# Kernel tuning notes

Hardware: AMD Instinct MI355X
Metric: run time of the kernel (lower is better)

Reference implementation:

```python
import jax, jax.numpy as jnp
import numpy as np

B, S, D_MODEL = 2, 2048, 2048
NUM_HEADS, NUM_KV_HEADS, HEAD_DIM = 16, 4, 128
MAX_SEQ = 2048
ROPE_WAVELENGTH = 10000.0


def apply_rope(x, positions, head_dim, max_wavelength):
    # x: [B, S, H, D], positions: [B, S]
    fraction = 2.0 * jnp.arange(0, head_dim // 2, dtype=jnp.float32) / head_dim
    timescale = max_wavelength ** fraction                      # [D/2]
    sinusoid = positions[..., None].astype(jnp.float32) / timescale  # [B,S,D/2]
    sin = jnp.sin(sinusoid)[:, :, None, :]                      # [B,S,1,D/2]
    cos = jnp.cos(sinusoid)[:, :, None, :]
    x1, x2 = jnp.split(x, 2, axis=-1)
    first = x1 * cos - x2 * sin
    second = x2 * cos + x1 * sin
    return jnp.concatenate([first, second], axis=-1).astype(x.dtype)


def setup_inputs() -> dict:
    key = jax.random.key(0)
    ks = jax.random.split(key, 5)
    inputs = jax.random.normal(ks[0], (B, S, D_MODEL), dtype=jnp.float32)
    seq_pos = jnp.broadcast_to(jnp.arange(S, dtype=jnp.int32)[None, :], (B, S))
    std = 0.01  # nnx.initializers.normal() default stddev
    wq = jax.random.normal(ks[1], (D_MODEL, NUM_HEADS, HEAD_DIM), dtype=jnp.float32) * std
    bq = jnp.zeros((NUM_HEADS, HEAD_DIM), dtype=jnp.float32)
    wkv = jax.random.normal(ks[2], (D_MODEL, NUM_KV_HEADS, 2 * HEAD_DIM), dtype=jnp.float32) * std
    bkv = jnp.zeros((NUM_KV_HEADS, 2 * HEAD_DIM), dtype=jnp.float32)
    wo = jax.random.normal(ks[3], (NUM_HEADS, HEAD_DIM, D_MODEL), dtype=jnp.float32) * std
    bo = jnp.zeros((D_MODEL,), dtype=jnp.float32)
    return {"inputs": inputs, "seq_pos": seq_pos, "wq": wq, "bq": bq,
            "wkv": wkv, "bkv": bkv, "wo": wo, "bo": bo}


def reference(inputs, seq_pos, wq, bq, wkv, bkv, wo, bo):
    dtype = inputs.dtype
    # Projections
    kv = jnp.einsum('bsd,dkh->bskh', inputs, wkv) + bkv          # [B,S,KV,2*HD]
    key, value = jnp.split(kv, 2, axis=-1)                       # [B,S,KV,HD] each
    query = jnp.einsum('bsd,dnh->bsnh', inputs, wq) + bq         # [B,S,H,HD]
    # RoPE
    query = apply_rope(query, seq_pos, HEAD_DIM, ROPE_WAVELENGTH)
    key = apply_rope(key, seq_pos, HEAD_DIM, ROPE_WAVELENGTH)
    # GQA: repeat KV heads
    rep = NUM_HEADS // NUM_KV_HEADS
    key_r = jnp.repeat(key, rep, axis=2)                          # [B,S,H,HD]
    value_r = jnp.repeat(value, rep, axis=2)
    # Attention (einsum_attention path)
    q = query / jnp.sqrt(jnp.asarray(HEAD_DIM, dtype=dtype))
    attn = jnp.einsum('bqhd,bkhd->bhqk', q, key_r)               # [B,H,S,S]
    # position_mask: seq_range <= time_steps -> causal
    seq_range = jnp.arange(MAX_SEQ, dtype=jnp.int32)
    mask = (seq_range[None, None, :] <= seq_pos[:, :, None])[:, None, :, :]  # [B,1,S,S]
    big_neg = jnp.finfo(dtype).min
    attn = jnp.where(mask, attn, big_neg)
    attn = jax.nn.softmax(attn, axis=-1).astype(dtype)
    x = jnp.einsum('bhqk,bkhd->bqhd', attn, value_r)             # [B,S,H,HD]
    out = jnp.einsum('bqhd,hdo->bqo', x, wo) + bo                # [B,S,D]
    return out
```

## Files before the change

### kernel.cpp

```cpp
#include <hip/hip_runtime.h>
#include <hip/hip_bf16.h>

#define DM    2048
#define SEQ   2048
#define NB    2
#define NH    16
#define NKVH  4
#define HD    128
#define NQKV  3072
#define MROWS 4096
#define KVB   64
#define QSC   0.08838834764831845f

using f32x4  = __attribute__((ext_vector_type(4))) float;
using f32x16 = __attribute__((ext_vector_type(16))) float;
using short8 = __attribute__((ext_vector_type(8))) short;
using ushort8 = __attribute__((ext_vector_type(8))) unsigned short;
using uint2v = __attribute__((ext_vector_type(2))) unsigned int;

static __device__ __forceinline__ unsigned short f2bf(float f) {
  __hip_bfloat16 h = __float2bfloat16(f);
  return *reinterpret_cast<unsigned short*>(&h);
}
static __device__ __forceinline__ float bf2f(unsigned short u) {
  union { unsigned int i; float f; } v; v.i = ((unsigned int)u) << 16; return v.f;
}
static __device__ __forceinline__ unsigned cvtpk_bf16(float lo, float hi) {
  unsigned r;
  asm("v_cvt_pk_bf16_f32 %0, %1, %2" : "=v"(r) : "v"(lo), "v"(hi));
  return r;
}

typedef __attribute__((address_space(1))) const unsigned char as1_c;
typedef __attribute__((address_space(3))) unsigned char as3_c;
static __device__ __forceinline__ void gload_lds16(const void* g, void* l) {
  __builtin_amdgcn_global_load_lds((as1_c*)g, (as3_c*)l, 16, 0, 0);
}


__global__ void build_trig(float2* __restrict__ tbl) {
  int i = blockIdx.x * 256 + threadIdx.x;
  int p = i >> 6, d = i & 63;
  float inv_ts = powf(10000.0f, -(float)d * (1.0f / 64.0f));
  float ang = (float)p * inv_ts;
  float sn, cs;
  sincosf(ang, &sn, &cs);
  tbl[i] = make_float2(cs, sn);
}


__global__ void f32_to_bf16_vec(const float* __restrict__ src, unsigned short* __restrict__ dst, int n4) {
  int i = blockIdx.x * blockDim.x + threadIdx.x;
  if (i < n4) {
    float4 v = reinterpret_cast<const float4*>(src)[i];
    ushort4 o;
    o.x = f2bf(v.x); o.y = f2bf(v.y); o.z = f2bf(v.z); o.w = f2bf(v.w);
    reinterpret_cast<ushort4*>(dst)[i] = o;
  }
}

__global__ void transpose_all(const float* __restrict__ wq, const float* __restrict__ wkv,
                              const float* __restrict__ wo,
                              unsigned short* __restrict__ WqkvT, unsigned short* __restrict__ WoT) {
  int bx = blockIdx.x;
  const float* src; unsigned short* dst; int N;
  if (bx < 64)       { src = wq;  dst = WqkvT;                         N = 2048; }
  else if (bx < 96)  { src = wkv; dst = WqkvT + (size_t)2048 * DM;     N = 1024; bx -= 64; }
  else               { src = wo;  dst = WoT;                           N = 2048; bx -= 96; }
  __shared__ float t[32][33];
  int n0 = bx * 32, k0 = blockIdx.y * 32;
  int tx = threadIdx.x, ty = threadIdx.y;
  for (int j = 0; j < 4; j++)
    t[ty + j * 8][tx] = src[(size_t)(k0 + ty + j * 8) * N + n0 + tx];
  __syncthreads();
  for (int j = 0; j < 4; j++)
    dst[(size_t)(n0 + ty + j * 8) * DM + k0 + tx] = f2bf(t[tx][ty + j * 8]);
}

__global__ void bias_concat(const float* __restrict__ bq, const float* __restrict__ bkv, float* __restrict__ o) {
  int i = blockIdx.x * 256 + threadIdx.x;
  if (i < NQKV) o[i] = (i < DM) ? bq[i] : bkv[i - DM];
}


#define STA(buf, kt, q) gload_lds16(gA + (size_t)((q) * 32) * K + (kt), LW + (buf) * 65536 + ((q) * 32 + rowA) * 128)
#define STB(buf, kt, h) gload_lds16(gB + (size_t)((h) * 64) * K + (kt), LW + (buf) * 65536 + 32768 + ((h) * 64 + rowB) * 128)

#define RDB(buf) \
  _Pragma("unroll") for (int ni = 0; ni < 4; ++ni) { \
    int row_ = (EPI == 1) ? (wc * 16 + ni * 64 + ln) : (wc * 64 + ni * 16 + ln); \
    const char* p_ = (const char*)LW + (buf) * 65536 + 32768 + row_ * 128; \
    bfr[ni][0] = *(const short8*)(p_ + coff0); \
    bfr[ni][1] = *(const short8*)(p_ + coff1); }

#define RDA(buf, q) \
  _Pragma("unroll") for (int m2 = 0; m2 < 2; ++m2) { \
    int row_ = wr * 128 + ((q) * 2 + m2) * 16 + ln; \
    const char* p_ = (const char*)LW + (buf) * 65536 + row_ * 128; \
    af[m2][0] = *(const short8*)(p_ + coff0); \
    af[m2][1] = *(const short8*)(p_ + coff1); }

#define MFQ(q) \
  _Pragma("unroll") for (int m2 = 0; m2 < 2; ++m2) \
  _Pragma("unroll") for (int ni = 0; ni < 4; ++ni) { \
    acc[(q) * 2 + m2][ni] = __builtin_amdgcn_mfma_f32_16x16x32_bf16(af[m2][0], bfr[ni][0], acc[(q) * 2 + m2][ni], 0, 0, 0); \
    acc[(q) * 2 + m2][ni] = __builtin_amdgcn_mfma_f32_16x16x32_bf16(af[m2][1], bfr[ni][1], acc[(q) * 2 + m2][ni], 0, 0, 0); }

#define SYNC_IN() do { __builtin_amdgcn_sched_barrier(0); __builtin_amdgcn_s_barrier(); \
  asm volatile("s_waitcnt lgkmcnt(0)" ::: "memory"); __builtin_amdgcn_sched_barrier(0); \
  __builtin_amdgcn_s_setprio(1); } while (0)
#define SYNC_OUT() do { __builtin_amdgcn_s_setprio(0); __builtin_amdgcn_sched_barrier(0); \
  __builtin_amdgcn_s_barrier(); } while (0)
#define SYNC_OUT_VM() do { __builtin_amdgcn_s_setprio(0); \
  asm volatile("s_waitcnt vmcnt(6)" ::: "memory"); __builtin_amdgcn_sched_barrier(0); \
  __builtin_amdgcn_s_barrier(); } while (0)

template <int EPI>
__global__ __launch_bounds__(512, 2) void gemm8(
    const unsigned short* __restrict__ A, const unsigned short* __restrict__ Bt,
    const float* __restrict__ bias, const int* __restrict__ seq_pos,
    const float2* __restrict__ tbl,
    unsigned short* __restrict__ Qo, unsigned short* __restrict__ Ko,
    unsigned short* __restrict__ Vo, float* __restrict__ Cout,
    int nbx, int N, int K) {
  __shared__ __align__(16) unsigned short lds[2 * 2 * 16384];
  int tid = threadIdx.x, lane = tid & 63, w = tid >> 6;
  int wr = w >> 2, wc = w & 3;
  int lg = lane >> 4, ln = lane & 15;

  int bid = blockIdx.x;
  int cpx = gridDim.x >> 3;
  int swz = (bid & 7) * cpx + (bid >> 3);
  int by = swz / nbx, bx = swz - by * nbx;
  int m0 = by * 256, n0 = bx * 256;

  int soff = ((lane & 7) ^ (lane >> 3)) << 3;
  const unsigned short* gA = A + (size_t)(m0 + ((w & 3) << 3) + ((w >> 2) << 7) + (lane >> 3)) * K + soff;
  const unsigned short* gB = Bt + (size_t)(n0 + (w << 3) + (lane >> 3)) * K + soff;
  char* LW = (char*)lds;
  int rowA = ((w & 3) << 3) + ((w >> 2) << 7);
  int rowB = (w << 3);
  int coff0 = ((lg)     ^ (ln & 7)) << 4;
  int coff1 = ((lg + 4) ^ (ln & 7)) << 4;

  f32x4 acc[8][4];
#pragma unroll
  for (int mi = 0; mi < 8; ++mi)
#pragma unroll
    for (int ni = 0; ni < 4; ++ni) acc[mi][ni] = (f32x4){0, 0, 0, 0};

  short8 bfr[4][2], af[2][2];

  STB(0, 0, 0); STB(0, 0, 1); STB(0, 0, 2); STB(0, 0, 3);
  STA(0, 0, 0); STA(0, 0, 1); STA(0, 0, 2); STA(0, 0, 3);
  STB(1, 64, 0); STB(1, 64, 1); STB(1, 64, 2); STB(1, 64, 3);
  STA(1, 64, 0); STA(1, 64, 1);
  asm volatile("s_waitcnt vmcnt(6)" ::: "memory");
  __builtin_amdgcn_sched_barrier(0);
  __builtin_amdgcn_s_barrier();

  for (int it = 0; it < (K >> 7); ++it) {
    int kt1  = it * 128 + 64;
    int ktn0 = (it * 128 + 128) & (K - 1);
    int ktn1 = (it * 128 + 192) & (K - 1);
    RDB(0); RDA(0, 0);
    STA(1, kt1, 2); STA(1, kt1, 3);
    SYNC_IN(); MFQ(0); SYNC_OUT();
    RDA(0, 1);
    STB(0, ktn0, 0); STB(0, ktn0, 1);
    SYNC_IN(); MFQ(1); SYNC_OUT();
    RDA(0, 2);
    STB(0, ktn0, 2); STB(0, ktn0, 3);
    SYNC_IN(); MFQ(2); SYNC_OUT();
    RDA(0, 3);
    STA(0, ktn0, 0); STA(0, ktn0, 1);
    SYNC_IN(); MFQ(3); SYNC_OUT_VM();
    RDB(1); RDA(1, 0);
    STA(0, ktn0, 2); STA(0, ktn0, 3);
    SYNC_IN(); MFQ(0); SYNC_OUT();
    RDA(1, 1);
    STB(1, ktn1, 0); STB(1, ktn1, 1);
    SYNC_IN(); MFQ(1); SYNC_OUT();
    RDA(1, 2);
    STB(1, ktn1, 2); STB(1, ktn1, 3);
    SYNC_IN(); MFQ(2); SYNC_OUT();
    RDA(1, 3);
    STA(1, ktn1, 0); STA(1, ktn1, 1);
    SYNC_IN(); MFQ(3); SYNC_OUT_VM();
  }
  asm volatile("s_waitcnt vmcnt(0)" ::: "memory");

  if constexpr (EPI == 0) {
#pragma unroll
    for (int mi = 0; mi < 8; ++mi) {
      int row = m0 + wr * 128 + mi * 16 + lg * 4;
#pragma unroll
      for (int ni = 0; ni < 4; ++ni) {
        int col = n0 + wc * 64 + ni * 16 + ln;
        float bv = bias[col];
#pragma unroll
        for (int r = 0; r < 4; ++r)
          Cout[(size_t)(row + r) * N + col] = acc[mi][ni][r] + bv;
      }
    }
  } else {
    int d = wc * 16 + ln;
    float bv0 = bias[n0 + d],      bv1 = bias[n0 + d + 64];
    float bv2 = bias[n0 + d + 128], bv3 = bias[n0 + d + 192];
    int bI = m0 >> 11, s0 = m0 & (SEQ - 1);
    int nt = n0 >> 8;
    if (nt < 8) {
      unsigned short* qp0 = Qo + (size_t)(bI * NH + nt * 2) * SEQ * HD;
      unsigned short* qp1 = qp0 + (size_t)SEQ * HD;
#pragma unroll
      for (int mi = 0; mi < 8; ++mi) {
        int sl = wr * 128 + mi * 16 + lg * 4;
#pragma unroll
        for (int r = 0; r < 4; ++r) {
          int s = s0 + sl + r;
          int pos = seq_pos[bI * SEQ + s];
          float2 cs = tbl[pos * 64 + d];
          float x1 = acc[mi][0][r] + bv0, x2 = acc[mi][1][r] + bv1;
          float y1 = acc[mi][2][r] + bv2, y2 = acc[mi][3][r] + bv3;
          unsigned short* q0 = qp0 + (size_t)s * HD;
          q0[d]      = f2bf((x1 * cs.x - x2 * cs.y) * QSC);
          q0[d + 64] = f2bf((x2 * cs.x + x1 * cs.y) * QSC);
          unsigned short* q1 = qp1 + (size_t)s * HD;
          q1[d]      = f2bf((y1 * cs.x - y2 * cs.y) * QSC);
          q1[d + 64] = f2bf((y2 * cs.x + y1 * cs.y) * QSC);
        }
      }
    } else {
      int kvh = nt - 8;
      unsigned short* kp = Ko + (size_t)(bI * NKVH + kvh) * SEQ * HD;
      unsigned short* vp = Vo + (size_t)(bI * NKVH + kvh) * HD * SEQ;
#pragma unroll
      for (int mi = 0; mi < 8; ++mi) {
        int sl = wr * 128 + mi * 16 + lg * 4;
        ushort4 v0q, v1q;
#pragma unroll
        for (int r = 0; r < 4; ++r) {
          int s = s0 + sl + r;
          int pos = seq_pos[bI * SEQ + s];
          float2 cs = tbl[pos * 64 + d];
          float x1 = acc[mi][0][r] + bv0, x2 = acc[mi][1][r] + bv1;
          unsigned short* krow = kp + (size_t)s * HD;
          krow[d]      = f2bf(x1 * cs.x - x2 * cs.y);
          krow[d + 64] = f2bf(x2 * cs.x + x1 * cs.y);
          ((unsigned short*)&v0q)[r] = f2bf(acc[mi][2][r] + bv2);
          ((unsigned short*)&v1q)[r] = f2bf(acc[mi][3][r] + bv3);
        }
        *(ushort4*)(vp + (size_t)d * SEQ + s0 + sl)        = v0q;
        *(ushort4*)(vp + (size_t)(d + 64) * SEQ + s0 + sl) = v1q;
      }
    }
  }
}


__global__ __launch_bounds__(256, 2) void flash_attn(const unsigned short* __restrict__ Q,
                                                     const unsigned short* __restrict__ Kr,
                                                     const unsigned short* __restrict__ Vt,
                                                     const int* __restrict__ seq_pos,
                                                     unsigned short* __restrict__ X) {
  __shared__ __align__(16) unsigned short lds_k[64 * 128];
  __shared__ __align__(16) unsigned short lds_v[128 * 64];
  int tid = threadIdx.x, lane = tid & 63, w = tid >> 6;
  int hi = lane >> 5, q5 = lane & 31;
  int bh = blockIdx.y, b = bh >> 4, h = bh & 15, kvhh = h >> 2;
  int qtile = 15 - (int)blockIdx.x;
  int qbase = qtile * 128;
  int q_global = qbase + w * 32 + q5;

  const unsigned short* kbase = Kr + ((size_t)(b * NKVH + kvhh)) * SEQ * HD;
  const unsigned short* vbase = Vt + ((size_t)(b * NKVH + kvhh)) * HD * SEQ;

  const unsigned short* gks[4]; unsigned short* lks[4];
  const unsigned short* gvs[4]; unsigned short* lvs[4];
#pragma unroll
  for (int i = 0; i < 4; i++) {
    int kr = w * 16 + i * 4 + (lane >> 4);
    int kc = (lane & 15) ^ (kr & 7);
    gks[i] = kbase + (size_t)kr * HD + kc * 8;
    lks[i] = lds_k + (w * 16 + i * 4) * 128;
    int vr = w * 32 + i * 8 + (lane >> 3);
    int vc = (lane & 7) ^ (vr & 7);
    gvs[i] = vbase + (size_t)vr * SEQ + vc * 8;
    lvs[i] = lds_v + (w * 32 + i * 8) * 64;
  }

  int pm = max(seq_pos[b * SEQ + qbase + lane], seq_pos[b * SEQ + qbase + 64 + lane]);
#pragma unroll
  for (int o = 32; o; o >>= 1) { int t2 = __shfl_xor(pm, o); pm = pm > t2 ? pm : t2; }
  int ntiles = (pm + KVB) >> 6;
  if (ntiles > SEQ / KVB) ntiles = SEQ / KVB;

  int pos_q = seq_pos[b * SEQ + q_global];
  int wmin = pos_q;
#pragma unroll
  for (int o = 32; o; o >>= 1) { int t2 = __shfl_xor(wmin, o); wmin = wmin < t2 ? wmin : t2; }

  short8 qf[8];
  {
    const unsigned short* qp = Q + ((size_t)((b * NH + h) * SEQ + q_global)) * HD + hi * 8;
#pragma unroll
    for (int c = 0; c < 8; c++) qf[c] = *reinterpret_cast<const short8*>(qp + c * 16);
  }

  f32x16 acc[4];
#pragma unroll
  for (int db = 0; db < 4; db++)
#pragma unroll
    for (int r = 0; r < 16; ++r) acc[db][r] = 0.0f;
  float m_q = -1e30f, l_q = 0.0f;

  const char* kp0 = (const char*)lds_k + q5 * 256;
  const char* kp1 = kp0 + 32 * 256;
  int swk = (q5 & 7) << 4;

  for (int t = 0; t < ntiles; t++) {
    int kv0 = t * KVB;
#pragma unroll
    for (int i = 0; i < 4; i++) {
      gload_lds16(gks[i] + (size_t)kv0 * HD, lks[i]);
      gload_lds16(gvs[i] + kv0, lvs[i]);
    }
    __syncthreads();

    f32x16 st0, st1;
#pragma unroll
    for (int r = 0; r < 16; ++r) { st0[r] = 0.0f; st1[r] = 0.0f; }
    __builtin_amdgcn_s_setprio(1);
#pragma unroll
    for (int c = 0; c < 8; c++) {
      short8 kf0 = *reinterpret_cast<const short8*>(kp0 + ((c * 32 + hi * 16) ^ swk));
      short8 kf1 = *reinterpret_cast<const short8*>(kp1 + ((c * 32 + hi * 16) ^ swk));
      st0 = __builtin_amdgcn_mfma_f32_32x32x16_bf16(kf0, qf[c], st0, 0, 0, 0);
      st1 = __builtin_amdgcn_mfma_f32_32x32x16_bf16(kf1, qf[c], st1, 0, 0, 0);
    }
    __builtin_amdgcn_s_setprio(0);

    if (kv0 + 63 > wmin) {
      int kvb = kv0 + 4 * hi;
#pragma unroll
      for (int r = 0; r < 16; ++r) {
        int kg = kvb + (r & 3) + 8 * (r >> 2);
        if (kg > pos_q)      st0[r] = -1e30f;
        if (kg + 32 > pos_q) st1[r] = -1e30f;
      }
    }

    float tm[16];
#pragma unroll
    for (int r = 0; r < 16; ++r) tm[r] = fmaxf(st0[r], st1[r]);
#pragma unroll
    for (int s = 8; s; s >>= 1)
#pragma unroll
      for (int r = 0; r < s; ++r) tm[r] = fmaxf(tm[r], tm[r + s]);
    float mx = fmaxf(tm[0], __shfl_xor(tm[0], 32));

    bool skip = (mx <= m_q + 8.0f) && (m_q > -1e29f);
    if (!__all((int)skip)) {
      float nm = fmaxf(m_q, mx);
      float corr = __expf(m_q - nm);
      m_q = nm; l_q *= corr;
#pragma unroll
      for (int db = 0; db < 4; db++)
#pragma unroll
        for (int r = 0; r < 16; ++r) acc[db][r] *= corr;
    }

    float sm[16];
#pragma unroll
    for (int r = 0; r < 16; ++r) {
      st0[r] = __expf(st0[r] - m_q);
      st1[r] = __expf(st1[r] - m_q);
      sm[r] = st0[r] + st1[r];
    }
#pragma unroll
    for (int s = 8; s; s >>= 1)
#pragma unroll
      for (int r = 0; r < s; ++r) sm[r] += sm[r + s];
    l_q += sm[0] + __shfl_xor(sm[0], 32);

    short8 pb[4];
#define MKFRAG(STV, B, OUT) { \
    unsigned a_ = cvtpk_bf16(STV[(B) + 0], STV[(B) + 1]); \
    unsigned b_ = cvtpk_bf16(STV[(B) + 2], STV[(B) + 3]); \
    unsigned c_ = cvtpk_bf16(STV[(B) + 4], STV[(B) + 5]); \
    unsigned d_ = cvtpk_bf16(STV[(B) + 6], STV[(B) + 7]); \
    uint2v r1_ = __builtin_amdgcn_permlane32_swap(a_, c_, false, false); \
    uint2v r2_ = __builtin_amdgcn_permlane32_swap(b_, d_, false, false); \
    union { unsigned u[4]; short8 s; } f_; \
    f_.u[0] = r1_[0]; f_.u[1] = r2_[0]; f_.u[2] = r1_[1]; f_.u[3] = r2_[1]; \
    OUT = f_.s; }
    MKFRAG(st0, 0, pb[0]);
    MKFRAG(st0, 8, pb[1]);
    MKFRAG(st1, 0, pb[2]);
    MKFRAG(st1, 8, pb[3]);
#undef MKFRAG

    __builtin_amdgcn_s_setprio(1);
#pragma unroll
    for (int db = 0; db < 4; db++) {
      const char* vr0 = (const char*)lds_v + (db * 32 + q5) * 128;
#pragma unroll
      for (int tt = 0; tt < 4; tt++) {
        short8 vf = *reinterpret_cast<const short8*>(vr0 + ((tt * 32 + hi * 16) ^ swk));
        acc[db] = __builtin_amdgcn_mfma_f32_32x32x16_bf16(vf, pb[tt], acc[db], 0, 0, 0);
      }
    }
    __builtin_amdgcn_s_setprio(0);
    __syncthreads();
  }

  float inv = l_q > 0.0f ? 1.0f / l_q : 0.0f;
  unsigned short* xp = X + ((size_t)(b * SEQ + q_global)) * DM + h * HD;
#pragma unroll
  for (int db = 0; db < 4; db++)
#pragma unroll
    for (int rq = 0; rq < 4; rq++) {
      int d = db * 32 + 4 * hi + 8 * rq;
      ushort4 o;
      unsigned short* op = (unsigned short*)&o;
#pragma unroll
      for (int j = 0; j < 4; j++) op[j] = f2bf(acc[db][rq * 4 + j] * inv);
      *(ushort4*)(xp + d) = o;
    }
}


extern "C" void kernel_launch(void* const* d_in, const int* in_sizes, int n_in,
                              void* d_out, int out_size, void* d_ws, size_t ws_size,
                              hipStream_t stream) {
  const float* inputs  = (const float*)d_in[0];
  const int*   seq_pos = (const int*)d_in[1];
  const float* wq  = (const float*)d_in[2];
  const float* bq  = (const float*)d_in[3];
  const float* wkv = (const float*)d_in[4];
  const float* bkv = (const float*)d_in[5];
  const float* wo  = (const float*)d_in[6];
  const float* bo  = (const float*)d_in[7];
  float* out = (float*)d_out;

  char* ws = (char*)d_ws;
  unsigned short* Abf     = (unsigned short*)(ws + 0);
  unsigned short* WqkvT   = (unsigned short*)(ws + 16777216);
  unsigned short* WoT     = (unsigned short*)(ws + 29360128);
  float*          biasqkv = (float*)(ws + 37748736);
  float2*         tbl     = (float2*)(ws + 37761024);
  unsigned short* Qr      = (unsigned short*)(ws + 38809600);
  unsigned short* Kr      = (unsigned short*)(ws + 55586816);
  unsigned short* Vt      = (unsigned short*)(ws + 59781120);
  unsigned short* Xb      = (unsigned short*)(ws + 63975424);

  build_trig<<<512, 256, 0, stream>>>(tbl);
  f32_to_bf16_vec<<<8192, 256, 0, stream>>>(inputs, Abf, (NB * SEQ * DM) / 4);
  transpose_all<<<dim3(160, 64), dim3(32, 8), 0, stream>>>(wq, wkv, wo, WqkvT, WoT);
  bias_concat<<<12, 256, 0, stream>>>(bq, bkv, biasqkv);

  gemm8<1><<<(MROWS / 256) * (NQKV / 256), 512, 0, stream>>>(
      Abf, WqkvT, biasqkv, seq_pos, tbl, Qr, Kr, Vt, nullptr, NQKV / 256, NQKV, DM);

  flash_attn<<<dim3(16, NB * NH), 256, 0, stream>>>(Qr, Kr, Vt, seq_pos, Xb);

  gemm8<0><<<(MROWS / 256) * (DM / 256), 512, 0, stream>>>(
      Xb, WoT, bo, nullptr, nullptr, nullptr, nullptr, nullptr, out, DM / 256, DM, DM);
}
```

Measured before the change: 308.8 us.

## Fuse preamble kernels, double-buffer flash-attn KV tiles, narrow output GEMM tiles

The four small setup kernels are merged into one preamble launch to cut launch overhead. Flash attention now double-buffers K/V tiles in LDS and prefetches two tiles ahead, so global loads overlap with compute instead of stalling each iteration. The output projection GEMM uses 256x128 tiles, giving 256 blocks instead of 128 to fill more CUs. This costs more LDS in attention, which may reduce occupancy, plus a separate pipeline schedule for the narrower GEMM.

Measured after the change: 293.5 us. 1.05x faster.

```diff
diff --git a/kernel.cpp b/kernel.cpp
--- a/kernel.cpp
+++ b/kernel.cpp
@@ -22,9 +22,6 @@
   __hip_bfloat16 h = __float2bfloat16(f);
   return *reinterpret_cast<unsigned short*>(&h);
 }
-static __device__ __forceinline__ float bf2f(unsigned short u) {
-  union { unsigned int i; float f; } v; v.i = ((unsigned int)u) << 16; return v.f;
-}
 static __device__ __forceinline__ unsigned cvtpk_bf16(float lo, float hi) {
   unsigned r;
   asm("v_cvt_pk_bf16_f32 %0, %1, %2" : "=v"(r) : "v"(lo), "v"(hi));
@@ -38,71 +35,69 @@
 }
 
 
-__global__ void build_trig(float2* __restrict__ tbl) {
-  int i = blockIdx.x * 256 + threadIdx.x;
-  int p = i >> 6, d = i & 63;
-  float inv_ts = powf(10000.0f, -(float)d * (1.0f / 64.0f));
-  float ang = (float)p * inv_ts;
-  float sn, cs;
-  sincosf(ang, &sn, &cs);
-  tbl[i] = make_float2(cs, sn);
-}
-
-
-__global__ void f32_to_bf16_vec(const float* __restrict__ src, unsigned short* __restrict__ dst, int n4) {
-  int i = blockIdx.x * blockDim.x + threadIdx.x;
-  if (i < n4) {
-    float4 v = reinterpret_cast<const float4*>(src)[i];
+__global__ __launch_bounds__(256) void preamble(
+    const float* __restrict__ inputs, const float* __restrict__ wq,
+    const float* __restrict__ wkv, const float* __restrict__ wo,
+    const float* __restrict__ bq, const float* __restrict__ bkv,
+    unsigned short* __restrict__ Abf, unsigned short* __restrict__ WqkvT,
+    unsigned short* __restrict__ WoT, float* __restrict__ biasqkv,
+    float2* __restrict__ tbl) {
+  int blk = blockIdx.x, tid = threadIdx.x;
+  if (blk < 8192) {
+    int i = blk * 256 + tid;
+    float4 v = reinterpret_cast<const float4*>(inputs)[i];
     ushort4 o;
     o.x = f2bf(v.x); o.y = f2bf(v.y); o.z = f2bf(v.z); o.w = f2bf(v.w);
-    reinterpret_cast<ushort4*>(dst)[i] = o;
-  }
-}
-
-__global__ void transpose_all(const float* __restrict__ wq, const float* __restrict__ wkv,
-                              const float* __restrict__ wo,
-                              unsigned short* __restrict__ WqkvT, unsigned short* __restrict__ WoT) {
-  int bx = blockIdx.x;
-  const float* src; unsigned short* dst; int N;
-  if (bx < 64)       { src = wq;  dst = WqkvT;                         N = 2048; }
-  else if (bx < 96)  { src = wkv; dst = WqkvT + (size_t)2048 * DM;     N = 1024; bx -= 64; }
-  else               { src = wo;  dst = WoT;                           N = 2048; bx -= 96; }
-  __shared__ float t[32][33];
-  int n0 = bx * 32, k0 = blockIdx.y * 32;
-  int tx = threadIdx.x, ty = threadIdx.y;
-  for (int j = 0; j < 4; j++)
-    t[ty + j * 8][tx] = src[(size_t)(k0 + ty + j * 8) * N + n0 + tx];
-  __syncthreads();
-  for (int j = 0; j < 4; j++)
-    dst[(size_t)(n0 + ty + j * 8) * DM + k0 + tx] = f2bf(t[tx][ty + j * 8]);
-}
-
-__global__ void bias_concat(const float* __restrict__ bq, const float* __restrict__ bkv, float* __restrict__ o) {
-  int i = blockIdx.x * 256 + threadIdx.x;
-  if (i < NQKV) o[i] = (i < DM) ? bq[i] : bkv[i - DM];
-}
-
-
-#define STA(buf, kt, q) gload_lds16(gA + (size_t)((q) * 32) * K + (kt), LW + (buf) * 65536 + ((q) * 32 + rowA) * 128)
-#define STB(buf, kt, h) gload_lds16(gB + (size_t)((h) * 64) * K + (kt), LW + (buf) * 65536 + 32768 + ((h) * 64 + rowB) * 128)
+    reinterpret_cast<ushort4*>(Abf)[i] = o;
+  } else if (blk < 18432) {
+    int rb = blk - 8192;
+    int bxx = rb % 160, byy = rb / 160;
+    const float* src; unsigned short* dst; int N;
+    if (bxx < 64)      { src = wq;  dst = WqkvT;                     N = 2048; }
+    else if (bxx < 96) { src = wkv; dst = WqkvT + (size_t)2048 * DM; N = 1024; bxx -= 64; }
+    else               { src = wo;  dst = WoT;                       N = 2048; bxx -= 96; }
+    __shared__ float t[32][33];
+    int n0 = bxx * 32, k0 = byy * 32;
+    int tx = tid & 31, ty = tid >> 5;
+    for (int j = 0; j < 4; j++)
+      t[ty + j * 8][tx] = src[(size_t)(k0 + ty + j * 8) * N + n0 + tx];
+    __syncthreads();
+    for (int j = 0; j < 4; j++)
+      dst[(size_t)(n0 + ty + j * 8) * DM + k0 + tx] = f2bf(t[tx][ty + j * 8]);
+  } else if (blk < 18944) {
+    int i = (blk - 18432) * 256 + tid;
+    int p = i >> 6, d = i & 63;
+    float inv_ts = powf(10000.0f, -(float)d * (1.0f / 64.0f));
+    float sn, cs;
+    sincosf((float)p * inv_ts, &sn, &cs);
+    tbl[i] = make_float2(cs, sn);
+  } else {
+    int i = (blk - 18944) * 256 + tid;
+    if (i < NQKV) biasqkv[i] = (i < DM) ? bq[i] : bkv[i - DM];
+  }
+}
+
+
+#define STA(buf, kt, q) gload_lds16(gA + (size_t)((q) * 32) * K + (kt), LW + (buf) * BUFB + ((q) * 32 + rowA) * 128)
+#define STB(buf, kt, h) gload_lds16(gB + (size_t)((h) * 64) * K + (kt), LW + (buf) * BUFB + 32768 + ((h) * 64 + rowB) * 128)
 
 #define RDB(buf) \
-  _Pragma("unroll") for (int ni = 0; ni < 4; ++ni) { \
-    int row_ = (EPI == 1) ? (wc * 16 + ni * 64 + ln) : (wc * 64 + ni * 16 + ln); \
-    const char* p_ = (const char*)LW + (buf) * 65536 + 32768 + row_ * 128; \
+  _Pragma("unroll") for (int ni = 0; ni < NIC; ++ni) { \
+    int row_ = (EPI == 1) ? (wc * 16 + ni * 64 + ln) : (wc * 16 * NIC + ni * 16 + ln); \
+    const char* p_ = (const char*)LW + (buf) * BUFB + 32768 + row_ * 128; \
     bfr[ni][0] = *(const short8*)(p_ + coff0); \
     bfr[ni][1] = *(const short8*)(p_ + coff1); }
 
 #define RDA(buf, q) \
   _Pragma("unroll") for (int m2 = 0; m2 < 2; ++m2) { \
     int row_ = wr * 128 + ((q) * 2 + m2) * 16 + ln; \
-    const char* p_ = (const char*)LW + (buf) * 65536 + row_ * 128; \
+    const char* p_ = (const char*)LW + (buf) * BUFB + row_ * 128; \
     af[m2][0] = *(const short8*)(p_ + coff0); \
     af[m2][1] = *(const short8*)(p_ + coff1); }
 
 #define MFQ(q) \
   _Pragma("unroll") for (int m2 = 0; m2 < 2; ++m2) \
-  _Pragma("unroll") for (int ni = 0; ni < 4; ++ni) { \
+  _Pragma("unroll") for (int ni = 0; ni < NIC; ++ni) { \
     acc[(q) * 2 + m2][ni] = __builtin_amdgcn_mfma_f32_16x16x32_bf16(af[m2][0], bfr[ni][0], acc[(q) * 2 + m2][ni], 0, 0, 0); \
     acc[(q) * 2 + m2][ni] = __builtin_amdgcn_mfma_f32_16x16x32_bf16(af[m2][1], bfr[ni][1], acc[(q) * 2 + m2][ni], 0, 0, 0); }
 
@@ -111,11 +106,14 @@
   __builtin_amdgcn_s_setprio(1); } while (0)
 #define SYNC_OUT() do { __builtin_amdgcn_s_setprio(0); __builtin_amdgcn_sched_barrier(0); \
   __builtin_amdgcn_s_barrier(); } while (0)
-#define SYNC_OUT_VM() do { __builtin_amdgcn_s_setprio(0); \
+#define SYNC_OUT_VM6() do { __builtin_amdgcn_s_setprio(0); \
   asm volatile("s_waitcnt vmcnt(6)" ::: "memory"); __builtin_amdgcn_sched_barrier(0); \
   __builtin_amdgcn_s_barrier(); } while (0)
-
-template <int EPI>
+#define SYNC_OUT_VM4() do { __builtin_amdgcn_s_setprio(0); \
+  asm volatile("s_waitcnt vmcnt(4)" ::: "memory"); __builtin_amdgcn_sched_barrier(0); \
+  __builtin_amdgcn_s_barrier(); } while (0)
+
+template <int EPI, int NIC>
 __global__ __launch_bounds__(512, 2) void gemm8(
     const unsigned short* __restrict__ A, const unsigned short* __restrict__ Bt,
     const float* __restrict__ bias, const int* __restrict__ seq_pos,
@@ -123,7 +121,8 @@
     unsigned short* __restrict__ Qo, unsigned short* __restrict__ Ko,
     unsigned short* __restrict__ Vo, float* __restrict__ Cout,
     int nbx, int N, int K) {
-  __shared__ __align__(16) unsigned short lds[2 * 2 * 16384];
+  constexpr int BUFB = 32768 + NIC * 8192;
+  __shared__ __align__(16) char lds[2 * BUFB];
   int tid = threadIdx.x, lane = tid & 63, w = tid >> 6;
   int wr = w >> 2, wc = w & 3;
   int lg = lane >> 4, ln = lane & 15;
@@ -132,7 +131,7 @@
   int cpx = gridDim.x >> 3;
   int swz = (bid & 7) * cpx + (bid >> 3);
   int by = swz / nbx, bx = swz - by * nbx;
-  int m0 = by * 256, n0 = bx * 256;
+  int m0 = by * 256, n0 = bx * (64 * NIC);
 
   int soff = ((lane & 7) ^ (lane >> 3)) << 3;
   const unsigned short* gA = A + (size_t)(m0 + ((w & 3) << 3) + ((w >> 2) << 7) + (lane >> 3)) * K + soff;
@@ -143,19 +142,27 @@
   int coff0 = ((lg)     ^ (ln & 7)) << 4;
   int coff1 = ((lg + 4) ^ (ln & 7)) << 4;
 
-  f32x4 acc[8][4];
+  f32x4 acc[8][NIC];
 #pragma unroll
   for (int mi = 0; mi < 8; ++mi)
 #pragma unroll
-    for (int ni = 0; ni < 4; ++ni) acc[mi][ni] = (f32x4){0, 0, 0, 0};
-
-  short8 bfr[4][2], af[2][2];
-
-  STB(0, 0, 0); STB(0, 0, 1); STB(0, 0, 2); STB(0, 0, 3);
-  STA(0, 0, 0); STA(0, 0, 1); STA(0, 0, 2); STA(0, 0, 3);
-  STB(1, 64, 0); STB(1, 64, 1); STB(1, 64, 2); STB(1, 64, 3);
-  STA(1, 64, 0); STA(1, 64, 1);
-  asm volatile("s_waitcnt vmcnt(6)" ::: "memory");
+    for (int ni = 0; ni < NIC; ++ni) acc[mi][ni] = (f32x4){0, 0, 0, 0};
+
+  short8 bfr[NIC][2], af[2][2];
+
+  if constexpr (NIC == 4) {
+    STB(0, 0, 0); STB(0, 0, 1); STB(0, 0, 2); STB(0, 0, 3);
+    STA(0, 0, 0); STA(0, 0, 1); STA(0, 0, 2); STA(0, 0, 3);
+    STB(1, 64, 0); STB(1, 64, 1); STB(1, 64, 2); STB(1, 64, 3);
+    STA(1, 64, 0); STA(1, 64, 1);
+    asm volatile("s_waitcnt vmcnt(6)" ::: "memory");
+  } else {
+    STB(0, 0, 0); STB(0, 0, 1);
+    STA(0, 0, 0); STA(0, 0, 1); STA(0, 0, 2); STA(0, 0, 3);
+    STB(1, 64, 0); STB(1, 64, 1);
+    STA(1, 64, 0); STA(1, 64, 1);
+    asm volatile("s_waitcnt vmcnt(4)" ::: "memory");
+  }
   __builtin_amdgcn_sched_barrier(0);
   __builtin_amdgcn_s_barrier();
 
@@ -163,30 +170,55 @@
     int kt1  = it * 128 + 64;
     int ktn0 = (it * 128 + 128) & (K - 1);
     int ktn1 = (it * 128 + 192) & (K - 1);
-    RDB(0); RDA(0, 0);
-    STA(1, kt1, 2); STA(1, kt1, 3);
-    SYNC_IN(); MFQ(0); SYNC_OUT();
-    RDA(0, 1);
-    STB(0, ktn0, 0); STB(0, ktn0, 1);
-    SYNC_IN(); MFQ(1); SYNC_OUT();
-    RDA(0, 2);
-    STB(0, ktn0, 2); STB(0, ktn0, 3);
-    SYNC_IN(); MFQ(2); SYNC_OUT();
-    RDA(0, 3);
-    STA(0, ktn0, 0); STA(0, ktn0, 1);
-    SYNC_IN(); MFQ(3); SYNC_OUT_VM();
-    RDB(1); RDA(1, 0);
-    STA(0, ktn0, 2); STA(0, ktn0, 3);
-    SYNC_IN(); MFQ(0); SYNC_OUT();
-    RDA(1, 1);
-    STB(1, ktn1, 0); STB(1, ktn1, 1);
-    SYNC_IN(); MFQ(1); SYNC_OUT();
-    RDA(1, 2);
-    STB(1, ktn1, 2); STB(1, ktn1, 3);
-    SYNC_IN(); MFQ(2); SYNC_OUT();
-    RDA(1, 3);
-    STA(1, ktn1, 0); STA(1, ktn1, 1);
-    SYNC_IN(); MFQ(3); SYNC_OUT_VM();
+    if constexpr (NIC == 4) {
+      RDB(0); RDA(0, 0);
+      STA(1, kt1, 2); STA(1, kt1, 3);
+      SYNC_IN(); MFQ(0); SYNC_OUT();
+      RDA(0, 1);
+      STB(0, ktn0, 0); STB(0, ktn0, 1);
+      SYNC_IN(); MFQ(1); SYNC_OUT();
+      RDA(0, 2);
+      STB(0, ktn0, 2); STB(0, ktn0, 3);
+      SYNC_IN(); MFQ(2); SYNC_OUT();
+      RDA(0, 3);
+      STA(0, ktn0, 0); STA(0, ktn0, 1);
+      SYNC_IN(); MFQ(3); SYNC_OUT_VM6();
+      RDB(1); RDA(1, 0);
+      STA(0, ktn0, 2); STA(0, ktn0, 3);
+      SYNC_IN(); MFQ(0); SYNC_OUT();
+      RDA(1, 1);
+      STB(1, ktn1, 0); STB(1, ktn1, 1);
+      SYNC_IN(); MFQ(1); SYNC_OUT();
+      RDA(1, 2);
+      STB(1, ktn1, 2); STB(1, ktn1, 3);
+      SYNC_IN(); MFQ(2); SYNC_OUT();
+      RDA(1, 3);
+      STA(1, ktn1, 0); STA(1, ktn1, 1);
+      SYNC_IN(); MFQ(3); SYNC_OUT_VM6();
+    } else {
+      RDB(0); RDA(0, 0);
+      STA(1, kt1, 2); STA(1, kt1, 3);
+      SYNC_IN(); MFQ(0); SYNC_OUT();
+      RDA(0, 1);
+      STB(0, ktn0, 0); STB(0, ktn0, 1);
+      SYNC_IN(); MFQ(1); SYNC_OUT();
+      RDA(0, 2);
+      STA(0, ktn0, 0); STA(0, ktn0, 1);
+      SYNC_IN(); MFQ(2); SYNC_OUT();
+      RDA(0, 3);
+      SYNC_IN(); MFQ(3); SYNC_OUT_VM4();
+      RDB(1); RDA(1, 0);
+      STA(0, ktn0, 2); STA(0, ktn0, 3);
+      SYNC_IN(); MFQ(0); SYNC_OUT();
+      RDA(1, 1);
+      STB(1, ktn1, 0); STB(1, ktn1, 1);
+      SYNC_IN(); MFQ(1); SYNC_OUT();
+      RDA(1, 2);
+      STA(1, ktn1, 0); STA(1, ktn1, 1);
+      SYNC_IN(); MFQ(2); SYNC_OUT();
+      RDA(1, 3);
+      SYNC_IN(); MFQ(3); SYNC_OUT_VM4();
+    }
   }
   asm volatile("s_waitcnt vmcnt(0)" ::: "memory");
 
@@ -195,8 +227,8 @@
     for (int mi = 0; mi < 8; ++mi) {
       int row = m0 + wr * 128 + mi * 16 + lg * 4;
 #pragma unroll
-      for (int ni = 0; ni < 4; ++ni) {
-        int col = n0 + wc * 64 + ni * 16 + ln;
+      for (int ni = 0; ni < NIC; ++ni) {
+        int col = n0 + wc * 16 * NIC + ni * 16 + ln;
         float bv = bias[col];
 #pragma unroll
         for (int r = 0; r < 4; ++r)
@@ -263,8 +295,8 @@
                                                      const unsigned short* __restrict__ Vt,
                                                      const int* __restrict__ seq_pos,
                                                      unsigned short* __restrict__ X) {
-  __shared__ __align__(16) unsigned short lds_k[64 * 128];
-  __shared__ __align__(16) unsigned short lds_v[128 * 64];
+  __shared__ __align__(16) unsigned short lds_k[2 * 64 * 128];
+  __shared__ __align__(16) unsigned short lds_v[2 * 128 * 64];
   int tid = threadIdx.x, lane = tid & 63, w = tid >> 6;
   int hi = lane >> 5, q5 = lane & 31;
   int bh = blockIdx.y, b = bh >> 4, h = bh & 15, kvhh = h >> 2;
@@ -289,6 +321,11 @@
     lvs[i] = lds_v + (w * 32 + i * 8) * 64;
   }
 
+#define ISSUE(t, buf) do { int kv0_ = (t) * KVB; \
+  _Pragma("unroll") for (int i_ = 0; i_ < 4; i_++) { \
+    gload_lds16(gks[i_] + (size_t)kv0_ * HD, lks[i_] + (buf) * 8192); \
+    gload_lds16(gvs[i_] + kv0_,              lvs[i_] + (buf) * 8192); } } while (0)
+
   int pm = max(seq_pos[b * SEQ + qbase + lane], seq_pos[b * SEQ + qbase + 64 + lane]);
 #pragma unroll
   for (int o = 32; o; o >>= 1) { int t2 = __shfl_xor(pm, o); pm = pm > t2 ? pm : t2; }
@@ -314,18 +351,21 @@
     for (int r = 0; r < 16; ++r) acc[db][r] = 0.0f;
   float m_q = -1e30f, l_q = 0.0f;
 
-  const char* kp0 = (const char*)lds_k + q5 * 256;
-  const char* kp1 = kp0 + 32 * 256;
   int swk = (q5 & 7) << 4;
 
+  ISSUE(0, 0);
+  ISSUE(1, 1);
+  asm volatile("s_waitcnt vmcnt(8)" ::: "memory");
+  __builtin_amdgcn_sched_barrier(0);
+  __syncthreads();
+
   for (int t = 0; t < ntiles; t++) {
+    int cur = t & 1;
     int kv0 = t * KVB;
-#pragma unroll
-    for (int i = 0; i < 4; i++) {
-      gload_lds16(gks[i] + (size_t)kv0 * HD, lks[i]);
-      gload_lds16(gvs[i] + kv0, lvs[i]);
-    }
-    __syncthreads();
+    const char* kb = (const char*)(lds_k + cur * 8192);
+    const char* vb = (const char*)(lds_v + cur * 8192);
+    const char* kp0 = kb + q5 * 256;
+    const char* kp1 = kp0 + 32 * 256;
 
     f32x16 st0, st1;
 #pragma unroll
@@ -403,7 +443,7 @@
     __builtin_amdgcn_s_setprio(1);
 #pragma unroll
     for (int db = 0; db < 4; db++) {
-      const char* vr0 = (const char*)lds_v + (db * 32 + q5) * 128;
+      const char* vr0 = vb + (db * 32 + q5) * 128;
 #pragma unroll
       for (int tt = 0; tt < 4; tt++) {
         short8 vf = *reinterpret_cast<const short8*>(vr0 + ((tt * 32 + hi * 16) ^ swk));
@@ -411,8 +451,18 @@
       }
     }
     __builtin_amdgcn_s_setprio(0);
+
     __syncthreads();
-  }
+    if (t + 2 < ntiles) {
+      ISSUE(t + 2, cur);
+      asm volatile("s_waitcnt vmcnt(8)" ::: "memory");
+    } else {
+      asm volatile("s_waitcnt vmcnt(0)" ::: "memory");
+    }
+    __builtin_amdgcn_sched_barrier(0);
+    __syncthreads();
+  }
+#undef ISSUE
 
   float inv = l_q > 0.0f ? 1.0f / l_q : 0.0f;
   unsigned short* xp = X + ((size_t)(b * SEQ + q_global)) * DM + h * HD;
@@ -454,16 +504,14 @@
   unsigned short* Vt      = (unsigned short*)(ws + 59781120);
   unsigned short* Xb      = (unsigned short*)(ws + 63975424);
 
-  build_trig<<<512, 256, 0, stream>>>(tbl);
-  f32_to_bf16_vec<<<8192, 256, 0, stream>>>(inputs, Abf, (NB * SEQ * DM) / 4);
-  transpose_all<<<dim3(160, 64), dim3(32, 8), 0, stream>>>(wq, wkv, wo, WqkvT, WoT);
-  bias_concat<<<12, 256, 0, stream>>>(bq, bkv, biasqkv);
-
-  gemm8<1><<<(MROWS / 256) * (NQKV / 256), 512, 0, stream>>>(
+  preamble<<<18956, 256, 0, stream>>>(inputs, wq, wkv, wo, bq, bkv,
+                                      Abf, WqkvT, WoT, biasqkv, tbl);
+
+  gemm8<1, 4><<<(MROWS / 256) * (NQKV / 256), 512, 0, stream>>>(
       Abf, WqkvT, biasqkv, seq_pos, tbl, Qr, Kr, Vt, nullptr, NQKV / 256, NQKV, DM);
 
   flash_attn<<<dim3(16, NB * NH), 256, 0, stream>>>(Qr, Kr, Vt, seq_pos, Xb);
 
-  gemm8<0><<<(MROWS / 256) * (DM / 256), 512, 0, stream>>>(
-      Xb, WoT, bo, nullptr, nullptr, nullptr, nullptr, nullptr, out, DM / 256, DM, DM);
-}
+  gemm8<0, 2><<<(MROWS / 256) * (DM / 128), 512, 0, stream>>>(
+      Xb, WoT, bo, nullptr, nullptr, nullptr, nullptr, nullptr, out, DM / 128, DM, DM);
+}
```
